# Kernel tuning notes

Hardware: AMD Instinct MI355X
Metric: run time of the kernel (lower is better)

The kernel has to match this reference:

```python
import jax, jax.numpy as jnp
import numpy as np

N_QUBITS = 9
N_CIR = 8
CHUNK = 256  # 2**(N_QUBITS-1)
DIM = 512    # 2**N_QUBITS

# Fixed gate sequence (kind, param_index, wires) transcribed from the qnode.
GATES = []
GATES += [("ry", i, (i,)) for i in range(9)]
GATES += [("rx", 9 + i, (i,)) for i in range(9)]
GATES += [("xx", 18 + k, w) for k, w in enumerate([(0,1),(8,7),(1,2),(7,6),(2,3),(6,5),(3,4),(5,4)])]
GATES += [("cry", 26 + k, w) for k, w in enumerate([(0,1),(1,2),(2,3),(8,7),(7,6),(6,5),(5,4),(3,4)])]
GATES += [("ry", 34 + i, (i,)) for i in range(9)]
GATES += [("xy", 43 + k, w) for k, w in enumerate([(4,3),(4,5),(3,2),(5,6),(2,1),(6,7),(1,0),(7,8)])]
GATES += [("crx", 51 + k, w) for k, w in enumerate([(0,1),(2,3),(5,6),(7,8),(1,2),(6,7)])]
GATES += [("rx", 57 + i, (i,)) for i in range(9)]
GATES += [("xx", 66 + k, w) for k, w in enumerate([(0,1),(8,7),(1,2),(7,6),(2,3),(6,5),(3,4),(5,4)])]
GATES += [("cry", 74 + k, w) for k, w in enumerate([(0,1),(1,2),(2,3),(8,7),(7,6),(6,5),(5,4),(3,4)])]
GATES += [("ry", 82 + i, (i,)) for i in range(9)]
GATES += [("xy", 91 + k, w) for k, w in enumerate([(4,3),(4,5),(3,2),(5,6),(2,1),(6,7),(1,0),(7,8)])]
GATES += [("crx", 99 + k, w) for k, w in enumerate([(0,1),(2,3),(5,6),(7,8),(1,2),(6,7)])]
GATES += [("rx", 105 + i, (i,)) for i in range(9)]
assert len(GATES) == 114

C64 = jnp.complex64

def _ry(t):
    c = jnp.cos(t / 2).astype(C64); s = jnp.sin(t / 2).astype(C64)
    return jnp.stack([jnp.stack([c, -s]), jnp.stack([s, c])])

def _rx(t):
    c = jnp.cos(t / 2).astype(C64); s = (-1j * jnp.sin(t / 2)).astype(C64)
    return jnp.stack([jnp.stack([c, s]), jnp.stack([s, c])])

def _xx(t):  # exp(-i t/2 XX)
    c = jnp.cos(t / 2).astype(C64); s = (-1j * jnp.sin(t / 2)).astype(C64)
    z = jnp.zeros_like(c)
    return jnp.stack([jnp.stack([c, z, z, s]), jnp.stack([z, c, s, z]),
                      jnp.stack([z, s, c, z]), jnp.stack([s, z, z, c])])

def _xy(t):  # PennyLane IsingXY
    c = jnp.cos(t / 2).astype(C64); s = (1j * jnp.sin(t / 2)).astype(C64)
    o = jnp.ones_like(c); z = jnp.zeros_like(c)
    return jnp.stack([jnp.stack([o, z, z, z]), jnp.stack([z, c, s, z]),
                      jnp.stack([z, s, c, z]), jnp.stack([z, z, z, o])])

def _ctrl(u2):  # block-diag(I2, u2): control on wires[0], target wires[1]
    z2 = jnp.zeros((2, 2), u2.dtype); i2 = jnp.eye(2, dtype=u2.dtype)
    return jnp.concatenate([jnp.concatenate([i2, z2], 1), jnp.concatenate([z2, u2], 1)], 0)

def _apply1(st, u, w):
    ax = 1 + w
    t = jnp.moveaxis(st, ax, -1)
    t = jnp.einsum('...a,ba->...b', t, u)
    return jnp.moveaxis(t, -1, ax)

def _apply2(st, u, w0, w1):
    a0, a1 = 1 + w0, 1 + w1
    t = jnp.moveaxis(st, (a0, a1), (-2, -1))
    sh = t.shape
    t = jnp.einsum('...a,ba->...b', t.reshape(sh[:-2] + (4,)), u).reshape(sh)
    return jnp.moveaxis(t, (-2, -1), (a0, a1))

def _circuit_probs(feats, qw):
    # feats: (N, 256) float32 -> analytic probs (N, 512)
    f = feats / jnp.linalg.norm(feats, axis=-1, keepdims=True)
    N = f.shape[0]
    # AmplitudeEmbedding on wires [0,1,2,3,5,6,7,8]; wire 4 stays |0>.
    st = jnp.stack([f.reshape(N, 16, 16), jnp.zeros((N, 16, 16), f.dtype)], axis=2)
    st = st.reshape((N,) + (2,) * N_QUBITS).astype(C64)
    for kind, idx, w in GATES:
        t = qw[idx]
        if kind == 'ry':
            st = _apply1(st, _ry(t), w[0])
        elif kind == 'rx':
            st = _apply1(st, _rx(t), w[0])
        elif kind == 'xx':
            st = _apply2(st, _xx(t), *w)
        elif kind == 'xy':
            st = _apply2(st, _xy(t), *w)
        elif kind == 'cry':
            st = _apply2(st, _ctrl(_ry(t)), *w)
        else:  # crx
            st = _apply2(st, _ctrl(_rx(t)), *w)
    return (st.real ** 2 + st.imag ** 2).reshape(N, DIM).astype(jnp.float32)


def setup_inputs() -> dict:
    key = jax.random.key(0)
    k1, k2 = jax.random.split(key)
    B = 4096
    return {
        "input_features": jax.random.normal(k1, (B, N_CIR * CHUNK), dtype=jnp.float32),
        "q_params": jax.random.normal(k2, (114,), dtype=jnp.float32),  # q_delta=1
    }


def reference(input_features, q_params):
    B = input_features.shape[0]
    q_in = jnp.tanh(input_features) * (np.pi / 2.0)
    chunks = q_in.reshape(B * N_CIR, CHUNK)          # per-sample split into 8 chunks of 256
    probs = _circuit_probs(chunks, q_params)          # (B*8, 512), all circuits batched
    return probs.reshape(B, 1024, 2, 2)
```

## Files before the change

kernel.cpp:

```cpp
#include <hip/hip_runtime.h>
#include <utility>

typedef __attribute__((ext_vector_type(8))) short short8;
typedef __attribute__((ext_vector_type(4))) float f32x4;
typedef unsigned short u16;

#define NROW 32768
#define KDIM 256
#define NOUT 512

static constexpr unsigned char cGK[114] = {
  0,0,0,0,0,0,0,0,0,
  1,1,1,1,1,1,1,1,1,
  2,2,2,2,2,2,2,2,
  4,4,4,4,4,4,4,4,
  0,0,0,0,0,0,0,0,0,
  3,3,3,3,3,3,3,3,
  5,5,5,5,5,5,
  1,1,1,1,1,1,1,1,1,
  2,2,2,2,2,2,2,2,
  4,4,4,4,4,4,4,4,
  0,0,0,0,0,0,0,0,0,
  3,3,3,3,3,3,3,3,
  5,5,5,5,5,5,
  1,1,1,1,1,1,1,1,1
};
static constexpr unsigned char cGW0[114] = {
  0,1,2,3,4,5,6,7,8,
  0,1,2,3,4,5,6,7,8,
  0,8,1,7,2,6,3,5,
  0,1,2,8,7,6,5,3,
  0,1,2,3,4,5,6,7,8,
  4,4,3,5,2,6,1,7,
  0,2,5,7,1,6,
  0,1,2,3,4,5,6,7,8,
  0,8,1,7,2,6,3,5,
  0,1,2,8,7,6,5,3,
  0,1,2,3,4,5,6,7,8,
  4,4,3,5,2,6,1,7,
  0,2,5,7,1,6,
  0,1,2,3,4,5,6,7,8
};
static constexpr unsigned char cGW1[114] = {
  0,0,0,0,0,0,0,0,0,
  0,0,0,0,0,0,0,0,0,
  1,7,2,6,3,5,4,4,
  1,2,3,7,6,5,4,4,
  0,0,0,0,0,0,0,0,0,
  3,5,2,6,1,7,0,8,
  1,3,6,8,2,7,
  0,0,0,0,0,0,0,0,0,
  1,7,2,6,3,5,4,4,
  1,2,3,7,6,5,4,4,
  0,0,0,0,0,0,0,0,0,
  3,5,2,6,1,7,0,8,
  1,3,6,8,2,7,
  0,0,0,0,0,0,0,0,0
};

__device__ __forceinline__ u16 f2bf(float f) {
  unsigned int u = __float_as_uint(f);
  u = (u + 0x7fffu + ((u >> 16) & 1u)) >> 16;
  return (u16)u;
}
__device__ __forceinline__ float bf2f(u16 b) {
  return __uint_as_float(((unsigned int)b) << 16);
}

typedef const __attribute__((address_space(1))) unsigned int* gptr_t;
typedef __attribute__((address_space(3))) unsigned int* lptr_t;
__device__ __forceinline__ void gload16(const void* g, void* l) {
  __builtin_amdgcn_global_load_lds((gptr_t)g, (lptr_t)l, 16, 0, 0);
}

template <int G>
__device__ __forceinline__ void apply_gate(float (&re)[8], float (&im)[8],
                                           float c0v, float s0v, float c1v,
                                           float s1v, int l) {
  constexpr int kind = cGK[G];
  constexpr int p0 = 8 - cGW0[G];
  constexpr int p1 = 8 - cGW1[G];
  constexpr int m = (kind <= 1) ? (1 << p0)
                  : (kind <= 3) ? ((1 << p0) | (1 << p1))
                  : (1 << p1);
  constexpr int ml = m & 63;
  constexpr int mr = m >> 6;
  float c = __shfl((G < 64) ? c0v : c1v, G & 63, 64);
  float s = __shfl((G < 64) ? s0v : s1v, G & 63, 64);
  float br[8], bi[8];
  #pragma unroll
  for (int r = 0; r < 8; ++r) { br[r] = re[r ^ mr]; bi[r] = im[r ^ mr]; }
  if constexpr (ml != 0) {
    #pragma unroll
    for (int r = 0; r < 8; ++r) {
      br[r] = __shfl_xor(br[r], ml, 64);
      bi[r] = __shfl_xor(bi[r], ml, 64);
    }
  }
  #pragma unroll
  for (int r = 0; r < 8; ++r) {
    const int idx = (r << 6) | l;
    float nre, nim;
    if constexpr (kind == 0) {
      float sg = ((idx >> p0) & 1) ? s : -s;
      nre = c * re[r] + sg * br[r];
      nim = c * im[r] + sg * bi[r];
    } else if constexpr (kind == 1 || kind == 2) {
      nre = c * re[r] + s * bi[r];
      nim = c * im[r] - s * br[r];
    } else if constexpr (kind == 3) {
      bool ap = (((idx >> p0) ^ (idx >> p1)) & 1) != 0;
      nre = ap ? (c * re[r] - s * bi[r]) : re[r];
      nim = ap ? (c * im[r] + s * br[r]) : im[r];
    } else if constexpr (kind == 4) {
      bool ap = ((idx >> p0) & 1) != 0;
      float sg = ((idx >> p1) & 1) ? s : -s;
      nre = ap ? (c * re[r] + sg * br[r]) : re[r];
      nim = ap ? (c * im[r] + sg * bi[r]) : im[r];
    } else {
      bool ap = ((idx >> p0) & 1) != 0;
      nre = ap ? (c * re[r] + s * bi[r]) : re[r];
      nim = ap ? (c * im[r] - s * br[r]) : im[r];
    }
    re[r] = nre; im[r] = nim;
  }
}

template <int... Gs>
__device__ __forceinline__ void apply_all(std::integer_sequence<int, Gs...>,
                                          float (&re)[8], float (&im)[8],
                                          float c0v, float s0v, float c1v,
                                          float s1v, int l) {
  (apply_gate<Gs>(re, im, c0v, s0v, c1v, s1v, l), ...);
}

__global__ void __launch_bounds__(256) prep_build(
    const float* __restrict__ x, const float* __restrict__ qp,
    u16* __restrict__ G, float* __restrict__ invn2, u16* __restrict__ BreT,
    u16* __restrict__ BimT) {
  int bid = blockIdx.x;
  int tid = threadIdx.x;
  int l = tid & 63;
  if (bid < 64) {
    int k = bid * 4 + (tid >> 6);
    float a0 = qp[l] * 0.5f;
    float a1 = (l < 50) ? qp[l + 64] * 0.5f : 0.f;
    float c0v = cosf(a0), s0v = sinf(a0);
    float c1v = cosf(a1), s1v = sinf(a1);

    int col = ((k >> 4) << 5) | (k & 15);
    float re[8], im[8];
    #pragma unroll
    for (int r = 0; r < 8; ++r) {
      re[r] = (r == (col >> 6) && l == (col & 63)) ? 1.f : 0.f;
      im[r] = 0.f;
    }
    apply_all(std::make_integer_sequence<int, 114>{}, re, im, c0v, s0v, c1v,
              s1v, l);
    #pragma unroll
    for (int r = 0; r < 8; ++r) {
      int j = (r << 6) | l;
      BreT[(size_t)j * KDIM + k] = f2bf(re[r]);
      BimT[(size_t)j * KDIM + k] = f2bf(im[r]);
    }
  } else {
    int gid = (bid - 64) * 256 + tid;
    int row = gid >> 6;
    const float H = 1.5707963267948966f;
    float4 v = *(const float4*)(x + ((size_t)row << 8) + l * 4);
    float g0 = tanhf(v.x) * H, g1 = tanhf(v.y) * H;
    float g2 = tanhf(v.z) * H, g3 = tanhf(v.w) * H;
    u16 b0 = f2bf(g0), b1 = f2bf(g1), b2 = f2bf(g2), b3 = f2bf(g3);
    float r0 = bf2f(b0), r1 = bf2f(b1), r2 = bf2f(b2), r3 = bf2f(b3);
    float sum = r0 * r0 + r1 * r1 + r2 * r2 + r3 * r3;
    #pragma unroll
    for (int o = 32; o; o >>= 1) sum += __shfl_xor(sum, o, 64);
    ushort4 pk; pk.x = b0; pk.y = b1; pk.z = b2; pk.w = b3;
    *(ushort4*)(G + ((size_t)row << 8) + l * 4) = pk;
    if (l == 0) invn2[row] = 1.0f / sum;
  }
}

__global__ void __launch_bounds__(256) gemm_probs(
    const u16* __restrict__ G, const u16* __restrict__ BreT,
    const u16* __restrict__ BimT, const float* __restrict__ invn2,
    float* __restrict__ out) {
  __shared__ __align__(16) char lds[32768];
  char* sA = lds;
  char* sBre = lds + 16384;
  char* sBim = lds + 24576;
  int tid = threadIdx.x;
  int l = tid & 63;
  int w = tid >> 6;
  int bid = blockIdx.x;
  int nw = (bid & 7) * 256 + (bid >> 3);
  int row0 = (nw >> 3) * 128;
  int n0 = (nw & 7) * 64;

  f32x4 accre[2][4] = {};
  f32x4 accim[2][4] = {};

  for (int k0 = 0; k0 < KDIM; k0 += 64) {
    __syncthreads();
    #pragma unroll
    for (int i = 0; i < 4; ++i) {
      int sg = w * 4 + i;
      int row = sg * 8 + (l >> 3);
      int chunk = (l & 7) ^ (row & 7);
      gload16(G + (size_t)(row0 + row) * KDIM + k0 + chunk * 8, sA + sg * 1024);
    }
    #pragma unroll
    for (int i = 0; i < 2; ++i) {
      int sg = w * 2 + i;
      int rn = sg * 8 + (l >> 3);
      int chunk = (l & 7) ^ (rn & 7);
      size_t off = (size_t)(n0 + rn) * KDIM + k0 + chunk * 8;
      gload16(BreT + off, sBre + sg * 1024);
      gload16(BimT + off, sBim + sg * 1024);
    }
    asm volatile("s_waitcnt vmcnt(0)" ::: "memory");
    __syncthreads();

    short8 aF[2][2], brF[4][2], biF[4][2];
    #pragma unroll
    for (int kk = 0; kk < 2; ++kk) {
      #pragma unroll
      for (int mr = 0; mr < 2; ++mr) {
        int row = w * 32 + mr * 16 + (l & 15);
        int chunk = (kk * 4 + (l >> 4)) ^ (row & 7);
        aF[mr][kk] = *(const short8*)(sA + row * 128 + chunk * 16);
      }
      #pragma unroll
      for (int nb = 0; nb < 4; ++nb) {
        int rn = nb * 16 + (l & 15);
        int chunk = (kk * 4 + (l >> 4)) ^ (rn & 7);
        brF[nb][kk] = *(const short8*)(sBre + rn * 128 + chunk * 16);
        biF[nb][kk] = *(const short8*)(sBim + rn * 128 + chunk * 16);
      }
    }
    #pragma unroll
    for (int kk = 0; kk < 2; ++kk)
      #pragma unroll
      for (int mr = 0; mr < 2; ++mr)
        #pragma unroll
        for (int nb = 0; nb < 4; ++nb) {
          accre[mr][nb] = __builtin_amdgcn_mfma_f32_16x16x32_bf16(
              aF[mr][kk], brF[nb][kk], accre[mr][nb], 0, 0, 0);
          accim[mr][nb] = __builtin_amdgcn_mfma_f32_16x16x32_bf16(
              aF[mr][kk], biF[nb][kk], accim[mr][nb], 0, 0, 0);
        }
  }

  #pragma unroll
  for (int mr = 0; mr < 2; ++mr) {
    int rbase = row0 + w * 32 + mr * 16 + (l >> 4) * 4;
    #pragma unroll
    for (int reg = 0; reg < 4; ++reg) {
      float inv = invn2[rbase + reg];
      #pragma unroll
      for (int nb = 0; nb < 4; ++nb) {
        float re = accre[mr][nb][reg];
        float im = accim[mr][nb][reg];
        __builtin_nontemporal_store(
            (re * re + im * im) * inv,
            out + (size_t)(rbase + reg) * NOUT + n0 + nb * 16 + (l & 15));
      }
    }
  }
}

extern "C" void kernel_launch(void* const* d_in, const int* in_sizes, int n_in,
                              void* d_out, int out_size, void* d_ws,
                              size_t ws_size, hipStream_t stream) {
  const float* x = (const float*)d_in[0];
  const float* qp = (const float*)d_in[1];
  float* out = (float*)d_out;
  char* ws = (char*)d_ws;
  u16* G = (u16*)ws;
  u16* BreT = (u16*)(ws + (16u << 20));
  u16* BimT = (u16*)(ws + (16u << 20) + (256u << 10));
  float* invn2 = (float*)(ws + (16u << 20) + (512u << 10));

  hipLaunchKernelGGL(prep_build, dim3(64 + NROW / 4), dim3(256), 0, stream, x,
                     qp, G, invn2, BreT, BimT);
  hipLaunchKernelGGL(gemm_probs, dim3((NROW / 128) * (NOUT / 64)), dim3(256),
                     0, stream, G, BreT, BimT, invn2, out);
}
```

Measured before the change: 55.20 us.

## Double-buffer LDS tiles in GEMM to overlap global loads with MFMA

Doubles the shared memory to 64KB and splits it into two buffers. The next K-tile is prefetched into one buffer while MFMA runs on the other, and the loop over the four K steps is fully unrolled. The goal is to hide global-to-LDS load latency behind compute and to drop one barrier per iteration. The larger LDS footprint may lower the number of blocks resident per CU.

```diff
diff --git a/kernel.cpp b/kernel.cpp
--- a/kernel.cpp
+++ b/kernel.cpp
@@ -185,10 +185,7 @@
     const u16* __restrict__ G, const u16* __restrict__ BreT,
     const u16* __restrict__ BimT, const float* __restrict__ invn2,
     float* __restrict__ out) {
-  __shared__ __align__(16) char lds[32768];
-  char* sA = lds;
-  char* sBre = lds + 16384;
-  char* sBim = lds + 24576;
+  __shared__ __align__(16) char lds[65536];
   int tid = threadIdx.x;
   int l = tid & 63;
   int w = tid >> 6;
@@ -200,56 +197,69 @@
   f32x4 accre[2][4] = {};
   f32x4 accim[2][4] = {};
 
-  for (int k0 = 0; k0 < KDIM; k0 += 64) {
-    __syncthreads();
-    #pragma unroll
-    for (int i = 0; i < 4; ++i) {
-      int sg = w * 4 + i;
-      int row = sg * 8 + (l >> 3);
-      int chunk = (l & 7) ^ (row & 7);
-      gload16(G + (size_t)(row0 + row) * KDIM + k0 + chunk * 8, sA + sg * 1024);
-    }
-    #pragma unroll
-    for (int i = 0; i < 2; ++i) {
-      int sg = w * 2 + i;
-      int rn = sg * 8 + (l >> 3);
-      int chunk = (l & 7) ^ (rn & 7);
-      size_t off = (size_t)(n0 + rn) * KDIM + k0 + chunk * 8;
-      gload16(BreT + off, sBre + sg * 1024);
-      gload16(BimT + off, sBim + sg * 1024);
-    }
-    asm volatile("s_waitcnt vmcnt(0)" ::: "memory");
-    __syncthreads();
-
-    short8 aF[2][2], brF[4][2], biF[4][2];
+  #define STAGE(bsel, k0)                                                    \
+    {                                                                        \
+      char* base_ = lds + (bsel) * 32768;                                    \
+      _Pragma("unroll") for (int i = 0; i < 4; ++i) {                        \
+        int sg = w * 4 + i;                                                  \
+        int row = sg * 8 + (l >> 3);                                         \
+        int chunk = (l & 7) ^ (row & 7);                                     \
+        gload16(G + (size_t)(row0 + row) * KDIM + (k0) + chunk * 8,          \
+                base_ + sg * 1024);                                          \
+      }                                                                      \
+      _Pragma("unroll") for (int i = 0; i < 2; ++i) {                        \
+        int sg = w * 2 + i;                                                  \
+        int rn = sg * 8 + (l >> 3);                                          \
+        int chunk = (l & 7) ^ (rn & 7);                                      \
+        size_t off = (size_t)(n0 + rn) * KDIM + (k0) + chunk * 8;            \
+        gload16(BreT + off, base_ + 16384 + sg * 1024);                      \
+        gload16(BimT + off, base_ + 24576 + sg * 1024);                      \
+      }                                                                      \
+    }
+
+  STAGE(0, 0);
+  asm volatile("s_waitcnt vmcnt(0)" ::: "memory");
+  __syncthreads();
+
+  #pragma unroll
+  for (int t = 0; t < 4; ++t) {
+    const int cur = t & 1;
+    if (t < 3) STAGE(cur ^ 1, (t + 1) * 64);
+    char* sA = lds + cur * 32768;
+    char* sBre = sA + 16384;
+    char* sBim = sA + 24576;
     #pragma unroll
     for (int kk = 0; kk < 2; ++kk) {
+      short8 aF[2], brF[4], biF[4];
       #pragma unroll
       for (int mr = 0; mr < 2; ++mr) {
         int row = w * 32 + mr * 16 + (l & 15);
         int chunk = (kk * 4 + (l >> 4)) ^ (row & 7);
-        aF[mr][kk] = *(const short8*)(sA + row * 128 + chunk * 16);
+        aF[mr] = *(const short8*)(sA + row * 128 + chunk * 16);
       }
       #pragma unroll
       for (int nb = 0; nb < 4; ++nb) {
         int rn = nb * 16 + (l & 15);
         int chunk = (kk * 4 + (l >> 4)) ^ (rn & 7);
-        brF[nb][kk] = *(const short8*)(sBre + rn * 128 + chunk * 16);
-        biF[nb][kk] = *(const short8*)(sBim + rn * 128 + chunk * 16);
+        brF[nb] = *(const short8*)(sBre + rn * 128 + chunk * 16);
+        biF[nb] = *(const short8*)(sBim + rn * 128 + chunk * 16);
       }
-    }
-    #pragma unroll
-    for (int kk = 0; kk < 2; ++kk)
       #pragma unroll
       for (int mr = 0; mr < 2; ++mr)
         #pragma unroll
         for (int nb = 0; nb < 4; ++nb) {
           accre[mr][nb] = __builtin_amdgcn_mfma_f32_16x16x32_bf16(
-              aF[mr][kk], brF[nb][kk], accre[mr][nb], 0, 0, 0);
+              aF[mr], brF[nb], accre[mr][nb], 0, 0, 0);
           accim[mr][nb] = __builtin_amdgcn_mfma_f32_16x16x32_bf16(
-              aF[mr][kk], biF[nb][kk], accim[mr][nb], 0, 0, 0);
+              aF[mr], biF[nb], accim[mr][nb], 0, 0, 0);
         }
-  }
+    }
+    if (t < 3) {
+      asm volatile("s_waitcnt vmcnt(0)" ::: "memory");
+      __syncthreads();
+    }
+  }
+  #undef STAGE
 
   #pragma unroll
   for (int mr = 0; mr < 2; ++mr) {
```

New measurement: 56.48 us. +2.3%, slower.

## Halve GEMM N-tile to 32 and remap blocks to XCD-local row panels

Applied to the files above, without the earlier changes.

Shrinks the per-block output tile from 128x64 to 128x32, doubling the grid to 4096 blocks and cutting LDS to 24KB and accumulator registers. It also changes the block-to-tile mapping so each XCD handles 32 contiguous row panels across all 16 column blocks, which aims to keep A panels resident in that XCD's L2. Fragment loads are also interleaved with the MFMA calls per k-step. The trade-off is that each A tile is now loaded from global memory twice as many times, and there is less MFMA work per LDS load, in exchange for higher occupancy and better cache locality.

```diff
diff --git a/kernel.cpp b/kernel.cpp
--- a/kernel.cpp
+++ b/kernel.cpp
@@ -185,20 +185,23 @@
     const u16* __restrict__ G, const u16* __restrict__ BreT,
     const u16* __restrict__ BimT, const float* __restrict__ invn2,
     float* __restrict__ out) {
-  __shared__ __align__(16) char lds[32768];
+  __shared__ __align__(16) char lds[24576];
   char* sA = lds;
   char* sBre = lds + 16384;
-  char* sBim = lds + 24576;
+  char* sBim = lds + 20480;
   int tid = threadIdx.x;
   int l = tid & 63;
   int w = tid >> 6;
   int bid = blockIdx.x;
-  int nw = (bid & 7) * 256 + (bid >> 3);
-  int row0 = (nw >> 3) * 128;
-  int n0 = (nw & 7) * 64;
-
-  f32x4 accre[2][4] = {};
-  f32x4 accim[2][4] = {};
+  int xcd = bid & 7;
+  int idx = bid >> 3;
+  int panel = xcd * 32 + (idx & 31);
+  int nblk = idx >> 5;
+  int row0 = panel * 128;
+  int n0 = nblk * 32;
+
+  f32x4 accre[2][2] = {};
+  f32x4 accim[2][2] = {};
 
   for (int k0 = 0; k0 < KDIM; k0 += 64) {
     __syncthreads();
@@ -209,46 +212,42 @@
       int chunk = (l & 7) ^ (row & 7);
       gload16(G + (size_t)(row0 + row) * KDIM + k0 + chunk * 8, sA + sg * 1024);
     }
-    #pragma unroll
-    for (int i = 0; i < 2; ++i) {
-      int sg = w * 2 + i;
-      int rn = sg * 8 + (l >> 3);
+    {
+      int rn = w * 8 + (l >> 3);
       int chunk = (l & 7) ^ (rn & 7);
       size_t off = (size_t)(n0 + rn) * KDIM + k0 + chunk * 8;
-      gload16(BreT + off, sBre + sg * 1024);
-      gload16(BimT + off, sBim + sg * 1024);
+      gload16(BreT + off, sBre + w * 1024);
+      gload16(BimT + off, sBim + w * 1024);
     }
     asm volatile("s_waitcnt vmcnt(0)" ::: "memory");
     __syncthreads();
 
-    short8 aF[2][2], brF[4][2], biF[4][2];
     #pragma unroll
     for (int kk = 0; kk < 2; ++kk) {
+      short8 aF[2], brF[2], biF[2];
       #pragma unroll
       for (int mr = 0; mr < 2; ++mr) {
         int row = w * 32 + mr * 16 + (l & 15);
         int chunk = (kk * 4 + (l >> 4)) ^ (row & 7);
-        aF[mr][kk] = *(const short8*)(sA + row * 128 + chunk * 16);
+        aF[mr] = *(const short8*)(sA + row * 128 + chunk * 16);
       }
       #pragma unroll
-      for (int nb = 0; nb < 4; ++nb) {
+      for (int nb = 0; nb < 2; ++nb) {
         int rn = nb * 16 + (l & 15);
         int chunk = (kk * 4 + (l >> 4)) ^ (rn & 7);
-        brF[nb][kk] = *(const short8*)(sBre + rn * 128 + chunk * 16);
-        biF[nb][kk] = *(const short8*)(sBim + rn * 128 + chunk * 16);
+        brF[nb] = *(const short8*)(sBre + rn * 128 + chunk * 16);
+        biF[nb] = *(const short8*)(sBim + rn * 128 + chunk * 16);
       }
-    }
-    #pragma unroll
-    for (int kk = 0; kk < 2; ++kk)
       #pragma unroll
       for (int mr = 0; mr < 2; ++mr)
         #pragma unroll
-        for (int nb = 0; nb < 4; ++nb) {
+        for (int nb = 0; nb < 2; ++nb) {
           accre[mr][nb] = __builtin_amdgcn_mfma_f32_16x16x32_bf16(
-              aF[mr][kk], brF[nb][kk], accre[mr][nb], 0, 0, 0);
+              aF[mr], brF[nb], accre[mr][nb], 0, 0, 0);
           accim[mr][nb] = __builtin_amdgcn_mfma_f32_16x16x32_bf16(
-              aF[mr][kk], biF[nb][kk], accim[mr][nb], 0, 0, 0);
+              aF[mr], biF[nb], accim[mr][nb], 0, 0, 0);
         }
+    }
   }
 
   #pragma unroll
@@ -258,7 +257,7 @@
     for (int reg = 0; reg < 4; ++reg) {
       float inv = invn2[rbase + reg];
       #pragma unroll
-      for (int nb = 0; nb < 4; ++nb) {
+      for (int nb = 0; nb < 2; ++nb) {
         float re = accre[mr][nb][reg];
         float im = accim[mr][nb][reg];
         __builtin_nontemporal_store(
@@ -283,6 +282,6 @@
 
   hipLaunchKernelGGL(prep_build, dim3(64 + NROW / 4), dim3(256), 0, stream, x,
                      qp, G, invn2, BreT, BimT);
-  hipLaunchKernelGGL(gemm_probs, dim3((NROW / 128) * (NOUT / 64)), dim3(256),
-                     0, stream, G, BreT, BimT, invn2, out);
-}
+  hipLaunchKernelGGL(gemm_probs, dim3(4096), dim3(256), 0, stream, G, BreT,
+                     BimT, invn2, out);
+}
```

Result: slower. 57.32 us (+3.8%).
